# Kernel tuning notes

Measured on AMD Instinct MI355X. Metric: run time of the kernel, lower is better.

## Reference

```python
import jax, jax.numpy as jnp
import numpy as np


def conv1x1(x, W, b):
    # x: [B,C,H,W], W: [O,C], b: [O]
    return jnp.einsum('bchw,oc->bohw', x, W) + b[None, :, None, None]


def setup_inputs() -> dict:
    key = jax.random.key(0)
    ks = jax.random.split(key, 16)
    B, C, H, W = 4, 256, 64, 64
    C4 = C // 4
    s = lambda fan_in: 1.0 / np.sqrt(fan_in)
    inp = {
        'last_frame': jax.random.normal(ks[0], (B, C, H, W), jnp.float32),
        'current_frame': jax.random.normal(ks[1], (B, C, H, W), jnp.float32),
        'future_frame': jax.random.normal(ks[2], (B, C, H, W), jnp.float32),
        'Wqk': jax.random.normal(ks[3], (C4, C), jnp.float32) * s(C),
        'bqk': jnp.zeros((C4,), jnp.float32),
        'Wkl': jax.random.normal(ks[4], (C4, C), jnp.float32) * s(C),
        'bkl': jnp.zeros((C4,), jnp.float32),
        'Wkf': jax.random.normal(ks[5], (C4, C), jnp.float32) * s(C),
        'bkf': jnp.zeros((C4,), jnp.float32),
        'Wv': jax.random.normal(ks[6], (C4, C), jnp.float32) * s(C),
        'bv': jnp.zeros((C4,), jnp.float32),
        'Wfire': jax.random.normal(ks[7], (C, C // 2), jnp.float32) * s(C // 2),
        'bfire': jnp.zeros((C,), jnp.float32),
        'bn_gamma': jnp.ones((C,), jnp.float32),
        'bn_beta': jnp.zeros((C,), jnp.float32),
        'bn_mean': jnp.zeros((C,), jnp.float32),
        'bn_var': jnp.ones((C,), jnp.float32),
    }
    return inp


def reference(last_frame, current_frame, future_frame,
              Wqk, bqk, Wkl, bkl, Wkf, bkf, Wv, bv,
              Wfire, bfire, bn_gamma, bn_beta, bn_mean, bn_var):
    B, C, H, W = current_frame.shape
    C4 = C // 4
    HW = H * W
    eps = 1e-5

    q = conv1x1(current_frame, Wqk, bqk).reshape(B, C4, HW)       # [B,C4,HW]
    kl = conv1x1(last_frame, Wkl, bkl).reshape(B, C4, HW)          # [B,C4,HW]
    kf = conv1x1(future_frame, Wkf, bkf).reshape(B, C4, HW)        # [B,C4,HW]
    v = conv1x1(current_frame, Wv, bv).reshape(B, C4, HW)          # [B,C4,HW]

    # affinity: [B, HW(query), HW(key)], softmax over key axis
    aff_l = jax.nn.softmax(jnp.einsum('bcq,bck->bqk', q, kl), axis=-1)
    aff_f = jax.nn.softmax(jnp.einsum('bcq,bck->bqk', q, kf), axis=-1)

    # out = V @ A^T : out[b,c,q] = sum_k v[b,c,k] * aff[b,q,k]
    out_l = jnp.einsum('bck,bqk->bcq', v, aff_l).reshape(B, C4, H, W)
    out_f = jnp.einsum('bck,bqk->bcq', v, aff_f).reshape(B, C4, H, W)

    fused = jnp.concatenate([out_l, out_f], axis=1)                 # [B,C/2,H,W]
    fired = conv1x1(fused, Wfire, bfire)                            # [B,C,H,W]
    # BatchNorm (inference form with running stats)
    inv = bn_gamma / jnp.sqrt(bn_var + eps)
    fired = fired * inv[None, :, None, None] + (bn_beta - bn_mean * inv)[None, :, None, None]
    return jax.nn.relu(current_frame + fired)
```

## Files before the change

kernel.cpp:

```cpp
#include <hip/hip_runtime.h>
#include <math.h>
#include <stdint.h>

#define HWN 4096
#define CIN 256
#define CQ 64
#define LOG2E 1.44269504f
#define C2OFF 56.0f

typedef __attribute__((ext_vector_type(8))) _Float16 f16x8;
typedef __attribute__((ext_vector_type(4))) _Float16 f16x4;
typedef __attribute__((ext_vector_type(8))) short    bf16x8;
typedef __attribute__((ext_vector_type(4))) short    bf16x4;
typedef __attribute__((ext_vector_type(4))) float    f32x4;

__device__ __forceinline__ short f2bf(float f) {
  union { float f; uint32_t u; } c; c.f = f;
  uint32_t r = (c.u + 0x7FFFu + ((c.u >> 16) & 1u)) >> 16;
  return (short)(uint16_t)r;
}

__device__ __forceinline__ void stage16(const void* g, void* l) {
  __builtin_amdgcn_global_load_lds(
      (const __attribute__((address_space(1))) uint32_t*)g,
      (__attribute__((address_space(3))) uint32_t*)l, 16, 0, 0);
}

__global__ __launch_bounds__(256) void prep_kernel(
    const float* __restrict__ Wqk, const float* __restrict__ Wkl,
    const float* __restrict__ Wkf, const float* __restrict__ Wv,
    const float* __restrict__ Wfire, const float* __restrict__ bfire,
    const float* __restrict__ gamma, const float* __restrict__ beta,
    const float* __restrict__ mean,  const float* __restrict__ var,
    _Float16* __restrict__ wqk_h, _Float16* __restrict__ wkl_h,
    _Float16* __restrict__ wkf_h, _Float16* __restrict__ wv_h,
    _Float16* __restrict__ wf_h, float* __restrict__ scale, float* __restrict__ shift) {
  int gid = blockIdx.x * 256 + threadIdx.x;
  if (gid < CQ * CIN) {
    wqk_h[gid] = (_Float16)(Wqk[gid] * LOG2E);
    wkl_h[gid] = (_Float16)Wkl[gid];
    wkf_h[gid] = (_Float16)Wkf[gid];
    wv_h[gid]  = (_Float16)Wv[gid];
  }
  if (gid < CIN * 128) wf_h[gid] = (_Float16)Wfire[gid];
  if (gid < CIN) {
    float inv = gamma[gid] / sqrtf(var[gid] + 1e-5f);
    scale[gid] = inv;
    shift[gid] = (bfire[gid] - mean[gid]) * inv + beta[gid];
  }
}

__global__ __launch_bounds__(256, 3) void proj_kernel(
    const float* __restrict__ cur, const float* __restrict__ last, const float* __restrict__ fut,
    const _Float16* __restrict__ wqk, const float* __restrict__ bqk,
    const _Float16* __restrict__ wkl, const float* __restrict__ bkl,
    const _Float16* __restrict__ wkf, const float* __restrict__ bkf,
    const _Float16* __restrict__ wv,  const float* __restrict__ bv,
    _Float16* __restrict__ q_out, _Float16* __restrict__ kl_out,
    _Float16* __restrict__ kf_out, short* __restrict__ v_out) {
  const int tid  = threadIdx.x;
  const int w    = tid >> 6;
  const int lane = tid & 63;
  const int quad = lane >> 4;
  const int l15  = lane & 15;
  const int pass = blockIdx.x >> 8;
  const int bb   = blockIdx.x & 255;
  const int b    = bb >> 6;
  const int hwt  = (bb & 63) << 6;
  const int hw   = hwt + w * 16 + l15;

  __shared__ __align__(16) _Float16 Tl[4][16][72];

  const float* X = (pass == 0) ? cur : ((pass == 1) ? last : fut);
  const float* xp = X + (size_t)b * CIN * HWN + hw;

  float xb[8][8];
#pragma unroll
  for (int c0 = 0; c0 < 8; ++c0)
#pragma unroll
    for (int j = 0; j < 8; ++j)
      xb[c0][j] = xp[(size_t)(c0 * 32 + quad * 8 + j) * HWN];

  if (pass == 0) {
    f32x4 aq[4] = {}; f32x4 av[4] = {};
#pragma unroll
    for (int k0 = 0; k0 < 8; ++k0) {
      f16x8 bh;
#pragma unroll
      for (int j = 0; j < 8; ++j) bh[j] = (_Float16)xb[k0][j];
#pragma unroll
      for (int mt = 0; mt < 4; ++mt) {
        f16x8 wa = *(const f16x8*)(wqk + (mt * 16 + l15) * CIN + k0 * 32 + quad * 8);
        aq[mt] = __builtin_amdgcn_mfma_f32_16x16x32_f16(wa, bh, aq[mt], 0, 0, 0);
        f16x8 wb = *(const f16x8*)(wv + (mt * 16 + l15) * CIN + k0 * 32 + quad * 8);
        av[mt] = __builtin_amdgcn_mfma_f32_16x16x32_f16(wb, bh, av[mt], 0, 0, 0);
      }
    }
#pragma unroll
    for (int mt = 0; mt < 4; ++mt)
#pragma unroll
      for (int r = 0; r < 4; ++r) {
        int oc = mt * 16 + quad * 4 + r;
        q_out[((size_t)b * CQ + oc) * HWN + hw] = (_Float16)(aq[mt][r] + bqk[oc] * LOG2E);
        v_out[((size_t)b * CQ + oc) * HWN + hw] = f2bf(av[mt][r] + bv[oc]);
      }
  } else {
    const _Float16* W = (pass == 1) ? wkl : wkf;
    const float* BI = (pass == 1) ? bkl : bkf;
    _Float16* OUT = (pass == 1) ? kl_out : kf_out;
    f32x4 a[4] = {};
#pragma unroll
    for (int k0 = 0; k0 < 8; ++k0) {
      f16x8 bh;
#pragma unroll
      for (int j = 0; j < 8; ++j) bh[j] = (_Float16)xb[k0][j];
#pragma unroll
      for (int mt = 0; mt < 4; ++mt) {
        f16x8 wa = *(const f16x8*)(W + (mt * 16 + l15) * CIN + k0 * 32 + quad * 8);
        a[mt] = __builtin_amdgcn_mfma_f32_16x16x32_f16(wa, bh, a[mt], 0, 0, 0);
      }
    }
#pragma unroll
    for (int mt = 0; mt < 4; ++mt) {
      f16x4 pw;
#pragma unroll
      for (int r = 0; r < 4; ++r)
        pw[r] = (_Float16)(a[mt][r] + BI[mt * 16 + quad * 4 + r]);
      *(f16x4*)&Tl[w][l15][mt * 16 + quad * 4] = pw;
    }
#pragma unroll
    for (int kk = 0; kk < 2; ++kk) {
      f16x8 row = *(const f16x8*)&Tl[w][l15][kk * 32 + quad * 8];
      *(f16x8*)(OUT + ((size_t)b * HWN + hw) * CQ + kk * 32 + quad * 8) = row;
    }
  }
}

__global__ __launch_bounds__(256, 2) void attn_kernel(
    const _Float16* __restrict__ qbuf, const _Float16* __restrict__ klbuf,
    const _Float16* __restrict__ kfbuf, const short* __restrict__ vbuf,
    _Float16* __restrict__ fused) {
  const int tid  = threadIdx.x;
  const int w    = tid >> 6;
  const int lane = tid & 63;
  const int quad = lane >> 4;
  const int l15  = lane & 15;

  const int xcd  = blockIdx.x & 7;
  const int L    = xcd * 64 + (blockIdx.x >> 3);
  const int qt   = (L & 63) << 6;
  const int pair = (L >> 6) & 1;
  const int b    = L >> 7;

  const int kh = w >> 1;
  const int wq = w & 1;

  const _Float16* K  = (pair ? kfbuf : klbuf) + (size_t)b * HWN * CQ;
  const short*    Vg = vbuf + (size_t)b * CQ * HWN;

  __shared__ __align__(16) _Float16 Kt[2][2][64][64];
  __shared__ __align__(16) short    Pl[4][32][72];

  const int qbase = qt + wq * 32;
  f16x8 qfrag[2][2];
#pragma unroll
  for (int qg = 0; qg < 2; ++qg)
#pragma unroll
    for (int kk = 0; kk < 2; ++kk)
#pragma unroll
      for (int j = 0; j < 8; ++j)
        qfrag[qg][kk][j] = qbuf[(b * CQ + kk * 32 + quad * 8 + j) * HWN +
                                qbase + qg * 16 + l15];

  f32x4 Oacc[2][4] = {};
  float psum[2] = {0.f, 0.f};

  const int swz  = (lane & 7) ^ ((lane >> 3) & 7);
  const int rswz = l15 & 7;

  const _Float16* ksrc =
      K + ((size_t)(kh * 32) * 64 + wq * 32 + (lane >> 3)) * CQ + swz * 8;
  const short* vsrc = Vg + (size_t)l15 * HWN + kh * 2048 + quad * 8;

  auto stageK = [&](int buf, int t) {
#pragma unroll
    for (int r = 0; r < 4; ++r)
      stage16(ksrc + ((size_t)t * 64 + r * 8) * CQ,
              &Kt[buf][kh][wq * 32 + r * 8][0]);
  };

  auto body = [&](int buf, int t) {
    bf16x8 vf[4][2];
#pragma unroll
    for (int ct = 0; ct < 4; ++ct)
#pragma unroll
      for (int kk = 0; kk < 2; ++kk)
        vf[ct][kk] = *(const bf16x8*)(vsrc + (size_t)ct * 16 * HWN + t * 64 + kk * 32);
    f16x8 kf[4][2];
#pragma unroll
    for (int nt = 0; nt < 4; ++nt)
#pragma unroll
      for (int kk = 0; kk < 2; ++kk)
        kf[nt][kk] = *(const f16x8*)&Kt[buf][kh][nt * 16 + l15][((kk * 4 + quad) ^ rswz) * 8];
#pragma unroll
    for (int qg = 0; qg < 2; ++qg) {
      f32x4 ST[4] = {};
      __builtin_amdgcn_s_setprio(1);
#pragma unroll
      for (int nt = 0; nt < 4; ++nt)
#pragma unroll
        for (int kk = 0; kk < 2; ++kk)
          ST[nt] = __builtin_amdgcn_mfma_f32_16x16x32_f16(kf[nt][kk], qfrag[qg][kk],
                                                          ST[nt], 0, 0, 0);
      __builtin_amdgcn_s_setprio(0);
#pragma unroll
      for (int nt = 0; nt < 4; ++nt) {
        bf16x4 pw;
#pragma unroll
        for (int r = 0; r < 4; ++r) {
          float p = __builtin_amdgcn_exp2f(ST[nt][r] - C2OFF);
          uint32_t u = __float_as_uint(p) & 0xffff0000u;
          psum[qg] += __uint_as_float(u);
          pw[r] = (short)(u >> 16);
        }
        *(bf16x4*)&Pl[w][qg * 16 + l15][nt * 16 + quad * 4] = pw;
      }
#pragma unroll
      for (int kk = 0; kk < 2; ++kk) {
        bf16x8 pf = *(const bf16x8*)&Pl[w][qg * 16 + l15][kk * 32 + quad * 8];
        __builtin_amdgcn_s_setprio(1);
#pragma unroll
        for (int ct = 0; ct < 4; ++ct)
          Oacc[qg][ct] = __builtin_amdgcn_mfma_f32_16x16x32_bf16(pf, vf[ct][kk],
                                                                 Oacc[qg][ct], 0, 0, 0);
        __builtin_amdgcn_s_setprio(0);
      }
    }
  };

  stageK(0, 0);
  __syncthreads();
#pragma unroll 1
  for (int tt = 0; tt < 32; tt += 2) {
    stageK(1, tt + 1);
    body(0, tt);
    __syncthreads();
    if (tt + 2 < 32) stageK(0, tt + 2);
    body(1, tt + 1);
    __syncthreads();
  }

#pragma unroll
  for (int qg = 0; qg < 2; ++qg) {
    psum[qg] += __shfl_xor(psum[qg], 16);
    psum[qg] += __shfl_xor(psum[qg], 32);
  }

  float* sc = (float*)&Kt[0][0][0][0];
  float* sp = sc + 4096;
  if (kh) {
#pragma unroll
    for (int qg = 0; qg < 2; ++qg) {
#pragma unroll
      for (int ct = 0; ct < 4; ++ct)
        *(f32x4*)&sc[((((wq * 2 + qg) * 4) + ct) << 8) + lane * 4] = Oacc[qg][ct];
      sp[(wq * 2 + qg) * 64 + lane] = psum[qg];
    }
  }
  __syncthreads();
  if (!kh) {
#pragma unroll
    for (int qg = 0; qg < 2; ++qg) {
      psum[qg] += sp[(wq * 2 + qg) * 64 + lane];
#pragma unroll
      for (int ct = 0; ct < 4; ++ct) {
        f32x4 o2 = *(const f32x4*)&sc[((((wq * 2 + qg) * 4) + ct) << 8) + lane * 4];
        Oacc[qg][ct] += o2;
      }
#pragma unroll
      for (int r = 0; r < 4; ++r) {
        float lt = __shfl(psum[qg], quad * 4 + r);
        float invl = __builtin_amdgcn_rcpf(lt);
        int qi = qbase + qg * 16 + quad * 4 + r;
#pragma unroll
        for (int ct = 0; ct < 4; ++ct)
          fused[((size_t)b * HWN + qi) * 128 + pair * 64 + ct * 16 + l15] =
              (_Float16)(Oacc[qg][ct][r] * invl);
      }
    }
  }
}

__global__ __launch_bounds__(256) void fire_kernel(
    const _Float16* __restrict__ fused, const _Float16* __restrict__ wf,
    const float* __restrict__ scale, const float* __restrict__ shift,
    const float* __restrict__ cur, float* __restrict__ out) {
  const int tid  = threadIdx.x;
  const int w    = tid >> 6;
  const int lane = tid & 63;
  const int quad = lane >> 4;
  const int l15  = lane & 15;
  const int g    = blockIdx.x & 3;
  const int bb   = blockIdx.x >> 2;
  const int b    = bb >> 6;
  const int hwt  = (bb & 63) << 6;
  const int hwb  = hwt + w * 16;

  f16x8 bfr[4];
#pragma unroll
  for (int k0 = 0; k0 < 4; ++k0)
    bfr[k0] = *(const f16x8*)(fused + ((size_t)b * HWN + hwb + l15) * 128 + k0 * 32 + quad * 8);

  float curv[4][4];
#pragma unroll
  for (int mt = 0; mt < 4; ++mt)
#pragma unroll
    for (int r = 0; r < 4; ++r)
      curv[mt][r] = cur[((size_t)b * CIN + g * 64 + mt * 16 + quad * 4 + r) * HWN + hwb + l15];

  f32x4 acc[4] = {};
#pragma unroll
  for (int k0 = 0; k0 < 4; ++k0)
#pragma unroll
    for (int mt = 0; mt < 4; ++mt) {
      f16x8 af = *(const f16x8*)(wf + (g * 64 + mt * 16 + l15) * 128 + k0 * 32 + quad * 8);
      acc[mt] = __builtin_amdgcn_mfma_f32_16x16x32_f16(af, bfr[k0], acc[mt], 0, 0, 0);
    }

#pragma unroll
  for (int mt = 0; mt < 4; ++mt)
#pragma unroll
    for (int r = 0; r < 4; ++r) {
      int oc = g * 64 + mt * 16 + quad * 4 + r;
      size_t idx = ((size_t)b * CIN + oc) * HWN + hwb + l15;
      float y = curv[mt][r] + acc[mt][r] * scale[oc] + shift[oc];
      out[idx] = fmaxf(y, 0.f);
    }
}

extern "C" void kernel_launch(void* const* d_in, const int* in_sizes, int n_in,
                              void* d_out, int out_size, void* d_ws, size_t ws_size,
                              hipStream_t stream) {
  const float* last  = (const float*)d_in[0];
  const float* cur   = (const float*)d_in[1];
  const float* fut   = (const float*)d_in[2];
  const float* Wqk   = (const float*)d_in[3];
  const float* bqk   = (const float*)d_in[4];
  const float* Wkl   = (const float*)d_in[5];
  const float* bkl   = (const float*)d_in[6];
  const float* Wkf   = (const float*)d_in[7];
  const float* bkf   = (const float*)d_in[8];
  const float* Wv    = (const float*)d_in[9];
  const float* bv    = (const float*)d_in[10];
  const float* Wfire = (const float*)d_in[11];
  const float* bfire = (const float*)d_in[12];
  const float* gamma = (const float*)d_in[13];
  const float* beta  = (const float*)d_in[14];
  const float* mean  = (const float*)d_in[15];
  const float* var   = (const float*)d_in[16];

  char* ws = (char*)d_ws;
  _Float16* qb     = (_Float16*)(ws);
  _Float16* klb    = (_Float16*)(ws + (2u << 20));
  _Float16* kfb    = (_Float16*)(ws + (4u << 20));
  short*    vb     = (short*)   (ws + (6u << 20));
  _Float16* fusedb = (_Float16*)(ws + (8u << 20));
  char* wsm = ws + (12u << 20);
  _Float16* wqk_h = (_Float16*)(wsm);
  _Float16* wkl_h = (_Float16*)(wsm + (32u << 10));
  _Float16* wkf_h = (_Float16*)(wsm + (64u << 10));
  _Float16* wv_h  = (_Float16*)(wsm + (96u << 10));
  _Float16* wf_h  = (_Float16*)(wsm + (128u << 10));
  float*    scale = (float*)   (wsm + (192u << 10));
  float*    shift = (float*)   (wsm + (193u << 10));
  float*    out   = (float*)d_out;

  prep_kernel<<<128, 256, 0, stream>>>(Wqk, Wkl, Wkf, Wv, Wfire, bfire,
                                       gamma, beta, mean, var,
                                       wqk_h, wkl_h, wkf_h, wv_h, wf_h, scale, shift);
  proj_kernel<<<768, 256, 0, stream>>>(cur, last, fut, wqk_h, bqk, wkl_h, bkl,
                                       wkf_h, bkf, wv_h, bv, qb, klb, kfb, vb);
  attn_kernel<<<512, 256, 0, stream>>>(qb, klb, kfb, vb, fusedb);
  fire_kernel<<<1024, 256, 0, stream>>>(fusedb, wf_h, scale, shift, cur, out);
}
```

Before: 214.4 us.

## Stage V tiles through LDS with async double-buffered loads alongside K

V fragments were loaded straight from global memory inside each loop body. They now go into a swizzled, double-buffered LDS tile via global_load_lds, issued one iteration ahead together with K, so global latency overlaps the MFMA work. The P scratch buffer is shrunk to one 16-row tile per wave and XOR-swizzled to reduce bank conflicts. In exchange, LDS use grows by 32KB, which may lower occupancy.

```diff
diff --git a/kernel.cpp b/kernel.cpp
--- a/kernel.cpp
+++ b/kernel.cpp
@@ -159,7 +159,8 @@
   const short*    Vg = vbuf + (size_t)b * CQ * HWN;
 
   __shared__ __align__(16) _Float16 Kt[2][2][64][64];
-  __shared__ __align__(16) short    Pl[4][32][72];
+  __shared__ __align__(16) short    Vt[2][2][64][64];
+  __shared__ __align__(16) short    Pl[4][16][64];
 
   const int qbase = qt + wq * 32;
   f16x8 qfrag[2][2];
@@ -179,8 +180,9 @@
   const int rswz = l15 & 7;
 
   const _Float16* ksrc =
-      K + ((size_t)(kh * 32) * 64 + wq * 32 + (lane >> 3)) * CQ + swz * 8;
-  const short* vsrc = Vg + (size_t)l15 * HWN + kh * 2048 + quad * 8;
+      K + ((size_t)(kh * 2048) + wq * 32 + (lane >> 3)) * CQ + swz * 8;
+  const short* vsrcS =
+      Vg + (size_t)(wq * 32 + (lane >> 3)) * HWN + kh * 2048 + swz * 8;
 
   auto stageK = [&](int buf, int t) {
 #pragma unroll
@@ -188,20 +190,26 @@
       stage16(ksrc + ((size_t)t * 64 + r * 8) * CQ,
               &Kt[buf][kh][wq * 32 + r * 8][0]);
   };
-
-  auto body = [&](int buf, int t) {
-    bf16x8 vf[4][2];
-#pragma unroll
-    for (int ct = 0; ct < 4; ++ct)
-#pragma unroll
-      for (int kk = 0; kk < 2; ++kk)
-        vf[ct][kk] = *(const bf16x8*)(vsrc + (size_t)ct * 16 * HWN + t * 64 + kk * 32);
+  auto stageV = [&](int buf, int t) {
+#pragma unroll
+    for (int r = 0; r < 4; ++r)
+      stage16(vsrcS + (size_t)(r * 8) * HWN + t * 64,
+              &Vt[buf][kh][wq * 32 + r * 8][0]);
+  };
+
+  auto body = [&](int buf) {
     f16x8 kf[4][2];
 #pragma unroll
     for (int nt = 0; nt < 4; ++nt)
 #pragma unroll
       for (int kk = 0; kk < 2; ++kk)
         kf[nt][kk] = *(const f16x8*)&Kt[buf][kh][nt * 16 + l15][((kk * 4 + quad) ^ rswz) * 8];
+    bf16x8 vf[4][2];
+#pragma unroll
+    for (int ct = 0; ct < 4; ++ct)
+#pragma unroll
+      for (int kk = 0; kk < 2; ++kk)
+        vf[ct][kk] = *(const bf16x8*)&Vt[buf][kh][ct * 16 + l15][((kk * 4 + quad) ^ rswz) * 8];
 #pragma unroll
     for (int qg = 0; qg < 2; ++qg) {
       f32x4 ST[4] = {};
@@ -223,11 +231,11 @@
           psum[qg] += __uint_as_float(u);
           pw[r] = (short)(u >> 16);
         }
-        *(bf16x4*)&Pl[w][qg * 16 + l15][nt * 16 + quad * 4] = pw;
+        *(bf16x4*)&Pl[w][l15][((nt * 2 + (quad >> 1)) ^ rswz) * 8 + (quad & 1) * 4] = pw;
       }
 #pragma unroll
       for (int kk = 0; kk < 2; ++kk) {
-        bf16x8 pf = *(const bf16x8*)&Pl[w][qg * 16 + l15][kk * 32 + quad * 8];
+        bf16x8 pf = *(const bf16x8*)&Pl[w][l15][((kk * 4 + quad) ^ rswz) * 8];
         __builtin_amdgcn_s_setprio(1);
 #pragma unroll
         for (int ct = 0; ct < 4; ++ct)
@@ -238,15 +246,15 @@
     }
   };
 
-  stageK(0, 0);
+  stageK(0, 0); stageV(0, 0);
   __syncthreads();
 #pragma unroll 1
   for (int tt = 0; tt < 32; tt += 2) {
-    stageK(1, tt + 1);
-    body(0, tt);
+    stageK(1, tt + 1); stageV(1, tt + 1);
+    body(0);
     __syncthreads();
-    if (tt + 2 < 32) stageK(0, tt + 2);
-    body(1, tt + 1);
+    if (tt + 2 < 32) { stageK(0, tt + 2); stageV(0, tt + 2); }
+    body(1);
     __syncthreads();
   }
 
```

New measurement: 200.5 us. 1.07x faster.
